# Performance work log

Hardware: AMD Instinct MI355X
Metric: run time of the kernel (lower is better)

## Reference

```python
import jax, jax.numpy as jnp
import numpy as np

B, N = 8192, 64
EPS = 1e-5
KARCHER_STEPS = 1


def _sym_apply(x, fn):
    # f(X) for symmetric X via eigendecomposition: V f(w) V^T
    w, v = jnp.linalg.eigh(x)
    return jnp.einsum('...ij,...j,...kj->...ik', v, fn(w), v)


def _logm(x):
    return _sym_apply(x, jnp.log)


def _expm(x):
    return _sym_apply(x, jnp.exp)


def sym_mat_pow(x, p):
    # X^p for SPD X, scalar (possibly traced) exponent p
    w, v = jnp.linalg.eigh(x)
    return jnp.einsum('...ij,...j,...kj->...ik', v, w ** p, v)


def _sqrt_and_invsqrt(m):
    # single eigh shared between m^{1/2} and m^{-1/2}
    w, v = jnp.linalg.eigh(m)
    sw = jnp.sqrt(w)
    s = jnp.einsum('...ij,...j,...kj->...ik', v, sw, v)
    si = jnp.einsum('...ij,...j,...kj->...ik', v, 1.0 / sw, v)
    return s, si


def karcher_flow(x, steps):
    # Frechet mean under AIRM via Karcher flow, init at arithmetic mean
    mean = x.mean(0)
    for _ in range(steps):
        s, si = _sqrt_and_invsqrt(mean)
        t = _logm(si @ x @ si).mean(0)  # mean tangent at current estimate
        mean = s @ _expm(t) @ s
    return mean


def batch_stats(x):
    mean = karcher_flow(x, KARCHER_STEPS)
    _, si = _sqrt_and_invsqrt(mean)
    logs = _logm(si @ x @ si)  # [B, n, n] tangent vectors at identity
    var = jnp.mean(jnp.sum(logs * logs, axis=(-2, -1)))  # mean squared AIRM distance
    return mean, jnp.sqrt(var)


def setup_inputs() -> dict:
    key = jax.random.key(0)
    k1, k2 = jax.random.split(key, 2)
    g = jax.random.normal(k1, (B, N, N), dtype=jnp.float32)
    x = g @ jnp.swapaxes(g, -1, -2) / N + 1e-3 * jnp.eye(N, dtype=jnp.float32)  # SPD batch
    h = jax.random.normal(k2, (N, N), dtype=jnp.float32)
    shift = h @ h.T / N + 0.1 * jnp.eye(N, dtype=jnp.float32)  # SPD shift parameter
    scale = jnp.ones((1,), dtype=jnp.float32)
    return {"x": x, "shift": shift, "scale": scale}


def reference(x, shift, scale):
    # batch stats are computed under no_grad in torch -> stop_gradient here
    mean, std = batch_stats(x)
    mean = jax.lax.stop_gradient(mean)
    std = jax.lax.stop_gradient(std)

    # parallel transport mean -> identity (whiten): mean^{-1/2} X mean^{-1/2}
    _, mi = _sqrt_and_invsqrt(mean)
    xw = mi @ x @ mi

    # scale by learnable scalar / batch std via matrix power
    p = (scale / (std + EPS))[0]
    y = sym_mat_pow(xw, p)

    # parallel transport identity -> shift: shift^{1/2} Y shift^{1/2}
    ss, _ = _sqrt_and_invsqrt(shift)
    return ss @ y @ ss
```

## Files before the change

### kernel.cpp

```cpp
#include <hip/hip_runtime.h>
#include <math.h>

#define ND 64
#define PAD 65
#define NN 4096
#define NB 8192

#define OFF_MEANPART ((size_t)0)
#define OFF_MEANA    ((size_t)131072)
#define OFF_S        ((size_t)135168)
#define OFF_SI       ((size_t)139264)
#define OFF_SS       ((size_t)143360)
#define OFF_TBAR     ((size_t)147456)
#define OFF_MI       ((size_t)151552)
#define OFF_P        ((size_t)155648)
#define OFF_VARPART  ((size_t)155712)
#define OFF_LAM      ((size_t)156736)
#define OFF_TPART    ((size_t)681024)

__device__ void jacobi2s(float (&A)[ND][PAD], float (&V)[ND][PAD], int tid) {
  __shared__ float cs_[32], sn_[32];
  __shared__ int   pp_[32], qq_[32];
  __shared__ int   rotcnt_;
  __shared__ float fro2_;
  __shared__ float red_[4];

  __syncthreads();
  float loc = 0.f;
  for (int e = tid; e < NN; e += 256) { float a = A[e >> 6][e & 63]; loc += a * a; }
  for (int o = 32; o; o >>= 1) loc += __shfl_down(loc, o);
  if ((tid & 63) == 0) red_[tid >> 6] = loc;
  __syncthreads();
  if (tid == 0) fro2_ = red_[0] + red_[1] + red_[2] + red_[3];
  __syncthreads();
  float fro2 = fro2_;

  for (int sweep = 0; sweep < 20; ++sweep) {
    if (tid == 0) rotcnt_ = 0;
    __syncthreads();
    for (int r = 0; r < 63; ++r) {
      if (tid < 32) {
        int p, q;
        if (tid == 0) { p = 63; q = r; }
        else { p = (r + tid) % 63; q = (r + 63 - tid) % 63; }
        if (p > q) { int t0 = p; p = q; q = t0; }
        pp_[tid] = p; qq_[tid] = q;
        float app = A[p][p], aqq = A[q][q], apq = A[p][q];
        float thr = fmaxf(1e-12f * fabsf(app * aqq), 1e-14f * fro2);
        float c = 1.f, s = 0.f;
        if (apq * apq > thr) {
          float tau = (aqq - app) / (2.f * apq);
          float t = 1.f / (fabsf(tau) + sqrtf(1.f + tau * tau));
          t = (tau < 0.f) ? -t : t;
          c = 1.f / sqrtf(1.f + t * t);
          s = t * c;
          atomicAdd(&rotcnt_, 1);
        }
        cs_[tid] = c; sn_[tid] = s;
      }
      __syncthreads();
      for (int t = tid; t < 2048; t += 256) {
        int k = t >> 6, j = t & 63;
        int p = pp_[k], q = qq_[k]; float c = cs_[k], s = sn_[k];
        float ap = A[p][j], aq = A[q][j];
        A[p][j] = c * ap - s * aq;
        A[q][j] = s * ap + c * aq;
      }
      __syncthreads();
      for (int t = tid; t < 4096; t += 256) {
        int k = (t >> 6) & 31, j = t & 63;
        int p = pp_[k], q = qq_[k]; float c = cs_[k], s = sn_[k];
        if (t < 2048) {
          float ap = A[j][p], aq = A[j][q];
          A[j][p] = c * ap - s * aq;
          A[j][q] = s * ap + c * aq;
        } else {
          float vp = V[j][p], vq = V[j][q];
          V[j][p] = c * vp - s * vq;
          V[j][q] = s * vp + c * vq;
        }
      }
      __syncthreads();
    }
    int rc = rotcnt_;
    __syncthreads();
    if (rc == 0) break;
  }
}

__device__ void recon_write(const float (&V)[ND][PAD], const float* f, float* g,
                            int c, int wq) {
  float acc[16];
#pragma unroll
  for (int k = 0; k < 16; ++k) acc[k] = 0.f;
  for (int j = 0; j < ND; ++j) {
    float m = f[j] * V[c][j];
#pragma unroll
    for (int k = 0; k < 16; ++k) acc[k] = fmaf(V[wq + 4 * k][j], m, acc[k]);
  }
#pragma unroll
  for (int k = 0; k < 16; ++k) g[(wq + 4 * k) * ND + c] = acc[k];
}

__device__ inline void jacobi1s(float (&w)[ND], int lane) {
  float g = 0.f;
#pragma unroll
  for (int i = 0; i < ND; ++i) g = fmaf(w[i], w[i], g);
  for (int sweep = 0; sweep < 18; ++sweep) {
    bool any = false;
    for (int r = 1; r < ND; ++r) {
      int partner = lane ^ r;
      float gv = __shfl(g, partner);
      float v[ND];
#pragma unroll
      for (int i = 0; i < ND; ++i) v[i] = __shfl(w[i], partner);
      float apq = 0.f;
#pragma unroll
      for (int i = 0; i < ND; ++i) apq = fmaf(w[i], v[i], apq);
      if (apq * apq > 4e-10f * g * gv) {
        bool amP = lane < partner;
        float app = amP ? g : gv;
        float aqq = amP ? gv : g;
        float tau = (aqq - app) / (2.f * apq);
        float t = 1.f / (fabsf(tau) + sqrtf(1.f + tau * tau));
        t = (tau < 0.f) ? -t : t;
        float c = 1.f / sqrtf(1.f + t * t);
        float s = t * c;
        float s2 = amP ? -s : s;
#pragma unroll
        for (int i = 0; i < ND; ++i) w[i] = fmaf(s2, v[i], c * w[i]);
        float d = t * apq;
        g = amP ? (g - d) : (g + d);
        any = true;
      }
    }
    if (!__any(any)) break;
  }
}


__global__ __launch_bounds__(256) void k_mean_part(const float* __restrict__ x,
                                                   float* __restrict__ part) {
  int e = blockIdx.x * 256 + threadIdx.x;
  int chunk = blockIdx.y;
  const float* px = x + (size_t)chunk * 256 * NN + e;
  float s = 0.f;
  for (int i = 0; i < 256; ++i) s += px[(size_t)i * NN];
  part[(size_t)chunk * NN + e] = s;
}

__global__ __launch_bounds__(256) void k_mean_final(const float* __restrict__ part,
                                                    float* __restrict__ meanA) {
  int e = blockIdx.x * 256 + threadIdx.x;
  float s = 0.f;
  for (int c = 0; c < 32; ++c) s += part[(size_t)c * NN + e];
  meanA[e] = s * (1.f / (float)NB);
}

__global__ __launch_bounds__(256) void k_prep1(const float* __restrict__ meanA,
                                               const float* __restrict__ shift,
                                               float* __restrict__ s_out,
                                               float* __restrict__ si_out,
                                               float* __restrict__ ss_out) {
  __shared__ float A[ND][PAD], V[ND][PAD];
  __shared__ float f1[ND], f2[ND];
  int tid = threadIdx.x;
  const float* src = (blockIdx.x == 0) ? meanA : shift;
  for (int e = tid; e < NN; e += 256) A[e >> 6][e & 63] = src[e];
  for (int e = tid; e < NN; e += 256) V[e >> 6][e & 63] = ((e >> 6) == (e & 63)) ? 1.f : 0.f;
  jacobi2s(A, V, tid);
  if (tid < ND) {
    float wv = fmaxf(A[tid][tid], 1e-30f);
    f1[tid] = sqrtf(wv);
    f2[tid] = 1.f / sqrtf(wv);
  }
  __syncthreads();
  int c = tid & 63, wq = tid >> 6;
  if (blockIdx.x == 0) {
    recon_write(V, f1, s_out, c, wq);
    recon_write(V, f2, si_out, c, wq);
  } else {
    recon_write(V, f1, ss_out, c, wq);
  }
}

__global__ __launch_bounds__(128, 2) void k_stage2(const float* __restrict__ x,
                                                   const float* __restrict__ si,
                                                   float* __restrict__ tPart,
                                                   int G2) {
  __shared__ float Xs[2][ND][PAD];
  __shared__ float lw_s[2][ND];
  int tid = threadIdx.x;
  int lane = tid & 63;
  int wv = tid >> 6;
  float (&X)[ND][PAD] = Xs[wv];
  int wid = blockIdx.x * 2 + wv;
  int nw = G2 * 2;

  float tacc[ND];
#pragma unroll
  for (int i2 = 0; i2 < ND; ++i2) tacc[i2] = 0.f;

  for (int i = wid; i < NB; i += nw) {
    for (int r2 = 0; r2 < ND; ++r2) X[r2][lane] = x[(size_t)i * NN + r2 * ND + lane];
    float w_[ND];
#pragma unroll
    for (int r2 = 0; r2 < ND; ++r2) w_[r2] = 0.f;
    for (int a = 0; a < ND; ++a) {
      float xa = X[a][lane];
#pragma unroll
      for (int r2 = 0; r2 < ND; ++r2) w_[r2] = fmaf(si[a * ND + r2], xa, w_[r2]);
    }
#pragma unroll
    for (int r2 = 0; r2 < ND; ++r2) X[r2][lane] = w_[r2];
#pragma unroll
    for (int r2 = 0; r2 < ND; ++r2) w_[r2] = 0.f;
    for (int a = 0; a < ND; ++a) {
      float sa = si[a * ND + lane];
#pragma unroll
      for (int r2 = 0; r2 < ND; ++r2) w_[r2] = fmaf(X[r2][a], sa, w_[r2]);
    }
    jacobi1s(w_, lane);
    float s2 = 0.f;
#pragma unroll
    for (int r2 = 0; r2 < ND; ++r2) s2 = fmaf(w_[r2], w_[r2], s2);
    float sig = sqrtf(fmaxf(s2, 1e-38f));
    float inv = 1.f / sig;
    lw_s[wv][lane] = logf(sig);
#pragma unroll
    for (int r2 = 0; r2 < ND; ++r2) X[r2][lane] = w_[r2] * inv;
    for (int j = 0; j < ND; ++j) {
      float m = lw_s[wv][j] * X[lane][j];
#pragma unroll
      for (int r2 = 0; r2 < ND; ++r2) tacc[r2] = fmaf(X[r2][j], m, tacc[r2]);
    }
  }
  if (wv == 1) {
#pragma unroll
    for (int r2 = 0; r2 < ND; ++r2) Xs[1][r2][lane] = tacc[r2];
  }
  __syncthreads();
  if (wv == 0) {
#pragma unroll
    for (int r2 = 0; r2 < ND; ++r2) tacc[r2] += Xs[1][r2][lane];
#pragma unroll
    for (int r2 = 0; r2 < ND; ++r2)
      tPart[(size_t)blockIdx.x * NN + r2 * ND + lane] = tacc[r2];
  }
}

__global__ __launch_bounds__(256) void k_reduce_t(const float* __restrict__ tPart,
                                                  float* __restrict__ tbar, int G2) {
  int e = blockIdx.x * 256 + threadIdx.x;
  float s = 0.f;
  for (int b = 0; b < G2; ++b) s += tPart[(size_t)b * NN + e];
  tbar[e] = s * (1.f / (float)NB);
}

__global__ __launch_bounds__(256) void k_prep2(const float* __restrict__ tbar,
                                               const float* __restrict__ s_g,
                                               float* __restrict__ mi_out) {
  __shared__ float A[ND][PAD], V[ND][PAD];
  __shared__ float f1[ND];
  int tid = threadIdx.x;
  int c = tid & 63, wq = tid >> 6;
  for (int e = tid; e < NN; e += 256) A[e >> 6][e & 63] = tbar[e];
  for (int e = tid; e < NN; e += 256) V[e >> 6][e & 63] = ((e >> 6) == (e & 63)) ? 1.f : 0.f;
  jacobi2s(A, V, tid);
  if (tid < ND) f1[tid] = expf(A[tid][tid]);
  __syncthreads();
  {
    float acc[16];
#pragma unroll
    for (int k = 0; k < 16; ++k) acc[k] = 0.f;
    for (int j = 0; j < ND; ++j) {
      float m = f1[j] * V[c][j];
#pragma unroll
      for (int k = 0; k < 16; ++k) acc[k] = fmaf(V[wq + 4 * k][j], m, acc[k]);
    }
    __syncthreads();
#pragma unroll
    for (int k = 0; k < 16; ++k) A[wq + 4 * k][c] = acc[k];
  }
  __syncthreads();
  {
    float acc[16];
#pragma unroll
    for (int k = 0; k < 16; ++k) acc[k] = 0.f;
    for (int a = 0; a < ND; ++a) {
      float ea = A[a][c];
#pragma unroll
      for (int k = 0; k < 16; ++k) acc[k] = fmaf(s_g[(wq + 4 * k) * ND + a], ea, acc[k]);
    }
    __syncthreads();
#pragma unroll
    for (int k = 0; k < 16; ++k) V[wq + 4 * k][c] = acc[k];
  }
  __syncthreads();
  {
    float acc[16];
#pragma unroll
    for (int k = 0; k < 16; ++k) acc[k] = 0.f;
    for (int a = 0; a < ND; ++a) {
      float sa = s_g[a * ND + c];
#pragma unroll
      for (int k = 0; k < 16; ++k) acc[k] = fmaf(V[wq + 4 * k][a], sa, acc[k]);
    }
    __syncthreads();
#pragma unroll
    for (int k = 0; k < 16; ++k) A[wq + 4 * k][c] = acc[k];
  }
  __syncthreads();
  for (int e = tid; e < NN; e += 256) V[e >> 6][e & 63] = ((e >> 6) == (e & 63)) ? 1.f : 0.f;
  jacobi2s(A, V, tid);
  if (tid < ND) f1[tid] = 1.f / sqrtf(fmaxf(A[tid][tid], 1e-30f));
  __syncthreads();
  recon_write(V, f1, mi_out, c, wq);
}

__global__ __launch_bounds__(128, 2) void k_stage3(const float* __restrict__ x,
                                                   const float* __restrict__ mi,
                                                   const float* __restrict__ ss,
                                                   float* __restrict__ aout,
                                                   float* __restrict__ lam,
                                                   float* __restrict__ varPart) {
  __shared__ float Xs[2][ND][PAD];
  __shared__ float vred[2];
  int tid = threadIdx.x;
  int lane = tid & 63;
  int wv = tid >> 6;
  float (&X)[ND][PAD] = Xs[wv];
  int wid = blockIdx.x * 2 + wv;
  int nw = gridDim.x * 2;
  float varacc = 0.f;

  for (int i = wid; i < NB; i += nw) {
    for (int r2 = 0; r2 < ND; ++r2) X[r2][lane] = x[(size_t)i * NN + r2 * ND + lane];
    float w_[ND];
#pragma unroll
    for (int r2 = 0; r2 < ND; ++r2) w_[r2] = 0.f;
    for (int a = 0; a < ND; ++a) {
      float xa = X[a][lane];
#pragma unroll
      for (int r2 = 0; r2 < ND; ++r2) w_[r2] = fmaf(mi[a * ND + r2], xa, w_[r2]);
    }
#pragma unroll
    for (int r2 = 0; r2 < ND; ++r2) X[r2][lane] = w_[r2];
#pragma unroll
    for (int r2 = 0; r2 < ND; ++r2) w_[r2] = 0.f;
    for (int a = 0; a < ND; ++a) {
      float sa = mi[a * ND + lane];
#pragma unroll
      for (int r2 = 0; r2 < ND; ++r2) w_[r2] = fmaf(X[r2][a], sa, w_[r2]);
    }
    jacobi1s(w_, lane);
    float s2 = 0.f;
#pragma unroll
    for (int r2 = 0; r2 < ND; ++r2) s2 = fmaf(w_[r2], w_[r2], s2);
    float sig = sqrtf(fmaxf(s2, 1e-38f));
    float inv = 1.f / sig;
    lam[(size_t)i * ND + lane] = sig;
    float lg = logf(sig);
    varacc = fmaf(lg, lg, varacc);
#pragma unroll
    for (int r2 = 0; r2 < ND; ++r2) X[r2][lane] = w_[r2] * inv;
    float acc[ND];
#pragma unroll
    for (int r2 = 0; r2 < ND; ++r2) acc[r2] = 0.f;
    for (int a = 0; a < ND; ++a) {
      float ua = X[a][lane];
#pragma unroll
      for (int r2 = 0; r2 < ND; ++r2) acc[r2] = fmaf(ss[a * ND + r2], ua, acc[r2]);
    }
#pragma unroll
    for (int r2 = 0; r2 < ND; ++r2)
      aout[(size_t)i * NN + r2 * ND + lane] = acc[r2];
  }
  for (int o = 32; o; o >>= 1) varacc += __shfl_down(varacc, o);
  if (lane == 0) vred[wv] = varacc;
  __syncthreads();
  if (tid == 0) varPart[blockIdx.x] = vred[0] + vred[1];
}

__global__ __launch_bounds__(64) void k_pfinal(const float* __restrict__ varPart,
                                               const float* __restrict__ scale,
                                               float* __restrict__ pout) {
  int tid = threadIdx.x;
  float s = 0.f;
  for (int i = tid; i < 1024; i += 64) s += varPart[i];
  for (int o = 32; o; o >>= 1) s += __shfl_down(s, o);
  if (tid == 0) {
    float var = s * (1.f / (float)NB);
    float sd = sqrtf(var);
    pout[0] = scale[0] / (sd + 1e-5f);
  }
}

__global__ __launch_bounds__(256) void k_stage5(const float* __restrict__ ain,
                                                const float* __restrict__ lam,
                                                const float* __restrict__ pws,
                                                float* __restrict__ out) {
  __shared__ float Ab[ND][PAD];
  __shared__ float lp[ND];
  int tid = threadIdx.x;
  int i = blockIdx.x;
  for (int e = tid; e < NN; e += 256) Ab[e >> 6][e & 63] = ain[(size_t)i * NN + e];
  if (tid < ND) {
    float p = pws[0];
    lp[tid] = powf(lam[(size_t)i * ND + tid], p);
  }
  __syncthreads();
  int c = tid & 63, wq = tid >> 6;
  float acc[16];
#pragma unroll
  for (int k = 0; k < 16; ++k) acc[k] = 0.f;
  for (int j = 0; j < ND; ++j) {
    float m = lp[j] * Ab[c][j];
#pragma unroll
    for (int k = 0; k < 16; ++k) acc[k] = fmaf(Ab[wq + 4 * k][j], m, acc[k]);
  }
#pragma unroll
  for (int k = 0; k < 16; ++k)
    out[(size_t)i * NN + (wq + 4 * k) * ND + c] = acc[k];
}

extern "C" void kernel_launch(void* const* d_in, const int* in_sizes, int n_in,
                              void* d_out, int out_size, void* d_ws, size_t ws_size,
                              hipStream_t stream) {
  const float* x     = (const float*)d_in[0];
  const float* shift = (const float*)d_in[1];
  const float* scale = (const float*)d_in[2];
  float* out = (float*)d_out;
  float* ws  = (float*)d_ws;
  (void)in_sizes; (void)n_in; (void)out_size;

  size_t wsf = ws_size / 4;
  int G2 = 1024;
  if (OFF_TPART + (size_t)G2 * NN > wsf) {
    size_t avail = (wsf > OFF_TPART) ? (wsf - OFF_TPART) / NN : 1;
    if (avail < 1) avail = 1;
    if (avail < (size_t)G2) G2 = (int)avail;
  }

  k_mean_part<<<dim3(16, 32), 256, 0, stream>>>(x, ws + OFF_MEANPART);
  k_mean_final<<<16, 256, 0, stream>>>(ws + OFF_MEANPART, ws + OFF_MEANA);
  k_prep1<<<2, 256, 0, stream>>>(ws + OFF_MEANA, shift, ws + OFF_S, ws + OFF_SI,
                                 ws + OFF_SS);
  k_stage2<<<G2, 128, 0, stream>>>(x, ws + OFF_SI, ws + OFF_TPART, G2);
  k_reduce_t<<<16, 256, 0, stream>>>(ws + OFF_TPART, ws + OFF_TBAR, G2);
  k_prep2<<<1, 256, 0, stream>>>(ws + OFF_TBAR, ws + OFF_S, ws + OFF_MI);
  k_stage3<<<1024, 128, 0, stream>>>(x, ws + OFF_MI, ws + OFF_SS, out,
                                     ws + OFF_LAM, ws + OFF_VARPART);
  k_pfinal<<<1, 64, 0, stream>>>(ws + OFF_VARPART, scale, ws + OFF_P);
  k_stage5<<<8192, 256, 0, stream>>>(out, ws + OFF_LAM, ws + OFF_P, out);
}
```

Before: 14.77 ms.

## Use DPP lane swaps in one-sided Jacobi and swizzled float4 shared-memory tiles

In the per-matrix one-sided Jacobi, each column-pair exchange now uses DPP row moves, permlane16 swaps and ds_bpermute in place of generic shuffles, and the dot product is split over four accumulators. The congruence transform and the log-reconstruction in stages 2 and 3 now load rows of x with float4 into an XOR-swizzled unpadded shared tile and read it back as float4. The goal is to cut shuffle latency in the hot Jacobi sweeps and reduce LDS bank conflicts and instruction count in the matrix products. In exchange the code is more complex, and it depends on a builtin that may be missing, in which case it falls back to bpermute.

Result: slower. 22.81 ms (+54.4%).

```diff
diff --git a/kernel.cpp b/kernel.cpp
--- a/kernel.cpp
+++ b/kernel.cpp
@@ -17,6 +17,27 @@
 #define OFF_VARPART  ((size_t)155712)
 #define OFF_LAM      ((size_t)156736)
 #define OFF_TPART    ((size_t)681024)
+
+typedef int v2i __attribute__((ext_vector_type(2)));
+
+template<int CTRL>
+__device__ __forceinline__ float dppf(float x) {
+  return __builtin_bit_cast(float,
+      __builtin_amdgcn_mov_dpp(__builtin_bit_cast(int, x), CTRL, 0xF, 0xF, true));
+}
+__device__ __forceinline__ float bperm_f(int pa, float x) {
+  return __builtin_bit_cast(float,
+      __builtin_amdgcn_ds_bpermute(pa, __builtin_bit_cast(int, x)));
+}
+#if __has_builtin(__builtin_amdgcn_permlane16_swap)
+#define HAVE_PL16 1
+__device__ __forceinline__ float pl16x(float x) {
+  int xi = __builtin_bit_cast(int, x);
+  v2i pr = __builtin_amdgcn_permlane16_swap(xi, xi, false, false);
+  unsigned r = (unsigned)pr.x + (unsigned)pr.y - (unsigned)xi;
+  return __builtin_bit_cast(float, (int)r);
+}
+#endif
 
 __device__ void jacobi2s(float (&A)[ND][PAD], float (&V)[ND][PAD], int tid) {
   __shared__ float cs_[32], sn_[32];
@@ -106,18 +127,70 @@
   float g = 0.f;
 #pragma unroll
   for (int i = 0; i < ND; ++i) g = fmaf(w[i], w[i], g);
+
   for (int sweep = 0; sweep < 18; ++sweep) {
     bool any = false;
     for (int r = 1; r < ND; ++r) {
-      int partner = lane ^ r;
-      float gv = __shfl(g, partner);
-      float v[ND];
-#pragma unroll
-      for (int i = 0; i < ND; ++i) v[i] = __shfl(w[i], partner);
-      float apq = 0.f;
-#pragma unroll
-      for (int i = 0; i < ND; ++i) apq = fmaf(w[i], v[i], apq);
+      float v[ND + 1];
+      if (r >= 32) {
+        int pa = ((lane ^ r) << 2);
+#pragma unroll
+        for (int i = 0; i < ND; ++i) v[i] = bperm_f(pa, w[i]);
+        v[ND] = bperm_f(pa, g);
+      } else {
+        switch (r & 3) {
+          case 0:
+#pragma unroll
+            for (int i = 0; i < ND; ++i) v[i] = w[i];
+            v[ND] = g;
+            break;
+          case 1:
+#pragma unroll
+            for (int i = 0; i < ND; ++i) v[i] = dppf<0xB1>(w[i]);
+            v[ND] = dppf<0xB1>(g);
+            break;
+          case 2:
+#pragma unroll
+            for (int i = 0; i < ND; ++i) v[i] = dppf<0x4E>(w[i]);
+            v[ND] = dppf<0x4E>(g);
+            break;
+          default:
+#pragma unroll
+            for (int i = 0; i < ND; ++i) v[i] = dppf<0x1B>(w[i]);
+            v[ND] = dppf<0x1B>(g);
+            break;
+        }
+        if (r & 4) {
+#pragma unroll
+          for (int i = 0; i <= ND; ++i) v[i] = dppf<0x1B>(dppf<0x141>(v[i]));
+        }
+        if (r & 8) {
+#pragma unroll
+          for (int i = 0; i <= ND; ++i) v[i] = dppf<0x141>(dppf<0x140>(v[i]));
+        }
+        if (r & 16) {
+#ifdef HAVE_PL16
+#pragma unroll
+          for (int i = 0; i <= ND; ++i) v[i] = pl16x(v[i]);
+#else
+          int pa16 = ((lane ^ 16) << 2);
+#pragma unroll
+          for (int i = 0; i <= ND; ++i) v[i] = bperm_f(pa16, v[i]);
+#endif
+        }
+      }
+      float gv = v[ND];
+      float a0 = 0.f, a1 = 0.f, a2 = 0.f, a3 = 0.f;
+#pragma unroll
+      for (int i = 0; i < ND; i += 4) {
+        a0 = fmaf(w[i + 0], v[i + 0], a0);
+        a1 = fmaf(w[i + 1], v[i + 1], a1);
+        a2 = fmaf(w[i + 2], v[i + 2], a2);
+        a3 = fmaf(w[i + 3], v[i + 3], a3);
+      }
+      float apq = (a0 + a1) + (a2 + a3);
       if (apq * apq > 4e-10f * g * gv) {
+        int partner = lane ^ r;
         bool amP = lane < partner;
         float app = amP ? g : gv;
         float aqq = amP ? gv : g;
@@ -138,6 +211,40 @@
   }
 }
 
+__device__ inline void congruence(const float* __restrict__ x_i,
+                                  const float* __restrict__ si,
+                                  float* __restrict__ XL, int lane,
+                                  float (&w_)[ND]) {
+#pragma unroll
+  for (int k = 0; k < 16; ++k) {
+    float4 rv = ((const float4*)(x_i + lane * ND))[k];
+    ((float4*)(XL + lane * ND))[k ^ (lane & 7)] = rv;
+  }
+  float B[ND];
+#pragma unroll
+  for (int i = 0; i < ND; ++i) B[i] = 0.f;
+  for (int a = 0; a < ND; ++a) {
+    float sa = si[a * ND + lane];
+    int ro = a * ND, sw = a & 7;
+#pragma unroll
+    for (int k = 0; k < 16; ++k) {
+      const float4 c4 = *((const float4*)(XL + ro + ((k ^ sw) << 2)));
+      B[4 * k + 0] = fmaf(c4.x, sa, B[4 * k + 0]);
+      B[4 * k + 1] = fmaf(c4.y, sa, B[4 * k + 1]);
+      B[4 * k + 2] = fmaf(c4.z, sa, B[4 * k + 2]);
+      B[4 * k + 3] = fmaf(c4.w, sa, B[4 * k + 3]);
+    }
+  }
+#pragma unroll
+  for (int a = 0; a < ND; ++a) XL[a * ND + lane] = B[a];
+#pragma unroll
+  for (int i = 0; i < ND; ++i) w_[i] = 0.f;
+  for (int a = 0; a < ND; ++a) {
+    float ba = XL[a * ND + lane];
+#pragma unroll
+    for (int r2 = 0; r2 < ND; ++r2) w_[r2] = fmaf(si[a * ND + r2], ba, w_[r2]);
+  }
+}
 
 __global__ __launch_bounds__(256) void k_mean_part(const float* __restrict__ x,
                                                    float* __restrict__ part) {
@@ -188,61 +295,58 @@
                                                    const float* __restrict__ si,
                                                    float* __restrict__ tPart,
                                                    int G2) {
-  __shared__ float Xs[2][ND][PAD];
-  __shared__ float lw_s[2][ND];
-  int tid = threadIdx.x;
-  int lane = tid & 63;
-  int wv = tid >> 6;
-  float (&X)[ND][PAD] = Xs[wv];
+  __shared__ float XLs[2][NN];
+  __shared__ float lws[2][ND];
+  int tid = threadIdx.x, lane = tid & 63, wv = tid >> 6;
+  float* XL = XLs[wv];
   int wid = blockIdx.x * 2 + wv;
   int nw = G2 * 2;
 
   float tacc[ND];
 #pragma unroll
-  for (int i2 = 0; i2 < ND; ++i2) tacc[i2] = 0.f;
+  for (int i = 0; i < ND; ++i) tacc[i] = 0.f;
 
   for (int i = wid; i < NB; i += nw) {
-    for (int r2 = 0; r2 < ND; ++r2) X[r2][lane] = x[(size_t)i * NN + r2 * ND + lane];
     float w_[ND];
-#pragma unroll
-    for (int r2 = 0; r2 < ND; ++r2) w_[r2] = 0.f;
-    for (int a = 0; a < ND; ++a) {
-      float xa = X[a][lane];
-#pragma unroll
-      for (int r2 = 0; r2 < ND; ++r2) w_[r2] = fmaf(si[a * ND + r2], xa, w_[r2]);
-    }
-#pragma unroll
-    for (int r2 = 0; r2 < ND; ++r2) X[r2][lane] = w_[r2];
-#pragma unroll
-    for (int r2 = 0; r2 < ND; ++r2) w_[r2] = 0.f;
-    for (int a = 0; a < ND; ++a) {
-      float sa = si[a * ND + lane];
-#pragma unroll
-      for (int r2 = 0; r2 < ND; ++r2) w_[r2] = fmaf(X[r2][a], sa, w_[r2]);
-    }
+    congruence(x + (size_t)i * NN, si, XL, lane, w_);
     jacobi1s(w_, lane);
     float s2 = 0.f;
 #pragma unroll
     for (int r2 = 0; r2 < ND; ++r2) s2 = fmaf(w_[r2], w_[r2], s2);
     float sig = sqrtf(fmaxf(s2, 1e-38f));
     float inv = 1.f / sig;
-    lw_s[wv][lane] = logf(sig);
-#pragma unroll
-    for (int r2 = 0; r2 < ND; ++r2) X[r2][lane] = w_[r2] * inv;
+    lws[wv][lane] = logf(sig);
+#pragma unroll
+    for (int k = 0; k < 16; ++k) {
+      float4 uv;
+      uv.x = w_[4 * k + 0] * inv;
+      uv.y = w_[4 * k + 1] * inv;
+      uv.z = w_[4 * k + 2] * inv;
+      uv.w = w_[4 * k + 3] * inv;
+      ((float4*)(XL + lane * ND))[k ^ (lane & 7)] = uv;
+    }
     for (int j = 0; j < ND; ++j) {
-      float m = lw_s[wv][j] * X[lane][j];
-#pragma unroll
-      for (int r2 = 0; r2 < ND; ++r2) tacc[r2] = fmaf(X[r2][j], m, tacc[r2]);
+      int ro = j * ND, sw = j & 7;
+      float uj = XL[ro + (((lane >> 2) ^ sw) << 2) + (lane & 3)];
+      float m = lws[wv][j] * uj;
+#pragma unroll
+      for (int k = 0; k < 16; ++k) {
+        const float4 c4 = *((const float4*)(XL + ro + ((k ^ sw) << 2)));
+        tacc[4 * k + 0] = fmaf(c4.x, m, tacc[4 * k + 0]);
+        tacc[4 * k + 1] = fmaf(c4.y, m, tacc[4 * k + 1]);
+        tacc[4 * k + 2] = fmaf(c4.z, m, tacc[4 * k + 2]);
+        tacc[4 * k + 3] = fmaf(c4.w, m, tacc[4 * k + 3]);
+      }
     }
   }
   if (wv == 1) {
 #pragma unroll
-    for (int r2 = 0; r2 < ND; ++r2) Xs[1][r2][lane] = tacc[r2];
+    for (int r2 = 0; r2 < ND; ++r2) XLs[1][r2 * ND + lane] = tacc[r2];
   }
   __syncthreads();
   if (wv == 0) {
 #pragma unroll
-    for (int r2 = 0; r2 < ND; ++r2) tacc[r2] += Xs[1][r2][lane];
+    for (int r2 = 0; r2 < ND; ++r2) tacc[r2] += XLs[1][r2 * ND + lane];
 #pragma unroll
     for (int r2 = 0; r2 < ND; ++r2)
       tPart[(size_t)blockIdx.x * NN + r2 * ND + lane] = tacc[r2];
@@ -324,35 +428,17 @@
                                                    float* __restrict__ aout,
                                                    float* __restrict__ lam,
                                                    float* __restrict__ varPart) {
-  __shared__ float Xs[2][ND][PAD];
+  __shared__ float XLs[2][NN];
   __shared__ float vred[2];
-  int tid = threadIdx.x;
-  int lane = tid & 63;
-  int wv = tid >> 6;
-  float (&X)[ND][PAD] = Xs[wv];
+  int tid = threadIdx.x, lane = tid & 63, wv = tid >> 6;
+  float* XL = XLs[wv];
   int wid = blockIdx.x * 2 + wv;
   int nw = gridDim.x * 2;
   float varacc = 0.f;
 
   for (int i = wid; i < NB; i += nw) {
-    for (int r2 = 0; r2 < ND; ++r2) X[r2][lane] = x[(size_t)i * NN + r2 * ND + lane];
     float w_[ND];
-#pragma unroll
-    for (int r2 = 0; r2 < ND; ++r2) w_[r2] = 0.f;
-    for (int a = 0; a < ND; ++a) {
-      float xa = X[a][lane];
-#pragma unroll
-      for (int r2 = 0; r2 < ND; ++r2) w_[r2] = fmaf(mi[a * ND + r2], xa, w_[r2]);
-    }
-#pragma unroll
-    for (int r2 = 0; r2 < ND; ++r2) X[r2][lane] = w_[r2];
-#pragma unroll
-    for (int r2 = 0; r2 < ND; ++r2) w_[r2] = 0.f;
-    for (int a = 0; a < ND; ++a) {
-      float sa = mi[a * ND + lane];
-#pragma unroll
-      for (int r2 = 0; r2 < ND; ++r2) w_[r2] = fmaf(X[r2][a], sa, w_[r2]);
-    }
+    congruence(x + (size_t)i * NN, mi, XL, lane, w_);
     jacobi1s(w_, lane);
     float s2 = 0.f;
 #pragma unroll
@@ -363,12 +449,12 @@
     float lg = logf(sig);
     varacc = fmaf(lg, lg, varacc);
 #pragma unroll
-    for (int r2 = 0; r2 < ND; ++r2) X[r2][lane] = w_[r2] * inv;
+    for (int a = 0; a < ND; ++a) XL[a * ND + lane] = w_[a] * inv;
     float acc[ND];
 #pragma unroll
     for (int r2 = 0; r2 < ND; ++r2) acc[r2] = 0.f;
     for (int a = 0; a < ND; ++a) {
-      float ua = X[a][lane];
+      float ua = XL[a * ND + lane];
 #pragma unroll
       for (int r2 = 0; r2 < ND; ++r2) acc[r2] = fmaf(ss[a * ND + r2], ua, acc[r2]);
     }
```

## Restructure per-matrix stages to one wave per block with swizzled LDS and bpermute Jacobi

Applied to the files above, without the earlier changes.

Stage 2 and stage 3 now run one 64-lane wave per block with twice as many blocks, each using a 16 KB unpadded LDS tile with an XOR swizzle so rows can be read and written as float4 without bank conflicts. The congruence products read the matrix in vectorized form and split accumulations across four FMA chains. The one-sided Jacobi sweep exchanges partner columns through ds_bpermute, with the norm folded into the same exchange, and returns the final column norm directly. Workspace offsets and the partial-reduction counts are adjusted for the larger grid. This adds more partial tiles to reduce and more LDS per block.

After: 16.29 ms. 10.3% more time.

```diff
diff --git a/kernel.cpp b/kernel.cpp
--- a/kernel.cpp
+++ b/kernel.cpp
@@ -15,8 +15,128 @@
 #define OFF_MI       ((size_t)151552)
 #define OFF_P        ((size_t)155648)
 #define OFF_VARPART  ((size_t)155712)
-#define OFF_LAM      ((size_t)156736)
-#define OFF_TPART    ((size_t)681024)
+#define OFF_LAM      ((size_t)157760)
+#define OFF_TPART    ((size_t)682048)
+
+#define G2_BLOCKS 2048
+#define G3_BLOCKS 2048
+
+__device__ __forceinline__ float bperm_f(int pa, float x) {
+  return __builtin_bit_cast(float,
+      __builtin_amdgcn_ds_bpermute(pa, __builtin_bit_cast(int, x)));
+}
+
+__device__ __forceinline__ constexpr int skey(int row) { return (row + (row >> 4)) & 15; }
+__device__ __forceinline__ int swz4(int row, int g) { return row * 64 + ((g ^ skey(row)) << 2); }
+__device__ __forceinline__ int swzE(int row, int e) {
+  return row * 64 + (((e >> 2) ^ skey(row)) << 2) + (e & 3);
+}
+
+__device__ float jacobi1s64(float (&w)[ND], int lane) {
+  float a0 = 0.f, a1 = 0.f, a2 = 0.f, a3 = 0.f;
+#pragma unroll
+  for (int i = 0; i < ND; i += 4) {
+    a0 = fmaf(w[i + 0], w[i + 0], a0);
+    a1 = fmaf(w[i + 1], w[i + 1], a1);
+    a2 = fmaf(w[i + 2], w[i + 2], a2);
+    a3 = fmaf(w[i + 3], w[i + 3], a3);
+  }
+  float g = (a0 + a1) + (a2 + a3);
+
+  for (int sweep = 0; sweep < 18; ++sweep) {
+    bool any = false;
+    for (int r = 1; r < ND; ++r) {
+      int pa = (lane ^ r) << 2;
+      float v[ND + 1];
+#pragma unroll
+      for (int i = 0; i <= ND; ++i) {
+        float t = bperm_f(pa, (i < ND) ? w[i] : g);
+        asm volatile("" : "+v"(t));
+        v[i] = t;
+      }
+      float gv = v[ND];
+      float b0 = 0.f, b1 = 0.f, b2 = 0.f, b3 = 0.f;
+#pragma unroll
+      for (int i = 0; i < ND; i += 4) {
+        b0 = fmaf(w[i + 0], v[i + 0], b0);
+        b1 = fmaf(w[i + 1], v[i + 1], b1);
+        b2 = fmaf(w[i + 2], v[i + 2], b2);
+        b3 = fmaf(w[i + 3], v[i + 3], b3);
+      }
+      float apq = (b0 + b1) + (b2 + b3);
+      if (apq * apq > 4e-10f * g * gv) {
+        int partner = lane ^ r;
+        bool amP = lane < partner;
+        float app = amP ? g : gv;
+        float aqq = amP ? gv : g;
+        float tau = (aqq - app) / (2.f * apq);
+        float t = 1.f / (fabsf(tau) + sqrtf(1.f + tau * tau));
+        t = (tau < 0.f) ? -t : t;
+        float c = 1.f / sqrtf(1.f + t * t);
+        float s = t * c;
+        float s2v = amP ? -s : s;
+#pragma unroll
+        for (int i = 0; i < ND; ++i) w[i] = fmaf(s2v, v[i], c * w[i]);
+        float d = t * apq;
+        g = amP ? (g - d) : (g + d);
+        any = true;
+      }
+    }
+    if (!__any(any)) break;
+  }
+  a0 = a1 = a2 = a3 = 0.f;
+#pragma unroll
+  for (int i = 0; i < ND; i += 4) {
+    a0 = fmaf(w[i + 0], w[i + 0], a0);
+    a1 = fmaf(w[i + 1], w[i + 1], a1);
+    a2 = fmaf(w[i + 2], w[i + 2], a2);
+    a3 = fmaf(w[i + 3], w[i + 3], a3);
+  }
+  return (a0 + a1) + (a2 + a3);
+}
+
+__device__ __forceinline__ void congruence1(const float* __restrict__ xi,
+                                            const float* __restrict__ q,
+                                            float* __restrict__ Xb, int lane,
+                                            float (&w)[ND]) {
+#pragma unroll
+  for (int k = 0; k < 16; ++k) {
+    int flat = k * 256 + lane * 4;
+    float4 rv = *(const float4*)(xi + flat);
+    int a = flat >> 6;
+    *(float4*)(Xb + swz4(a, lane & 15)) = rv;
+  }
+  __syncthreads();
+  float B[ND];
+#pragma unroll
+  for (int r = 0; r < ND; ++r) B[r] = 0.f;
+  const float* qc = q + lane * ND;
+  for (int a = 0; a < ND; ++a) {
+    float sa = qc[a];
+#pragma unroll
+    for (int g2 = 0; g2 < 16; ++g2) {
+      float4 xa = *(const float4*)(Xb + swz4(a, g2));
+      B[4 * g2 + 0] = fmaf(xa.x, sa, B[4 * g2 + 0]);
+      B[4 * g2 + 1] = fmaf(xa.y, sa, B[4 * g2 + 1]);
+      B[4 * g2 + 2] = fmaf(xa.z, sa, B[4 * g2 + 2]);
+      B[4 * g2 + 3] = fmaf(xa.w, sa, B[4 * g2 + 3]);
+    }
+  }
+  __syncthreads();
+#pragma unroll
+  for (int g2 = 0; g2 < 16; ++g2) {
+    float4 b4 = make_float4(B[4 * g2 + 0], B[4 * g2 + 1], B[4 * g2 + 2], B[4 * g2 + 3]);
+    *(float4*)(Xb + swz4(lane, g2)) = b4;
+  }
+#pragma unroll
+  for (int r = 0; r < ND; ++r) w[r] = 0.f;
+  for (int a = 0; a < ND; ++a) {
+    float ba = Xb[swzE(lane, a)];
+    const float* qr = q + a * ND;
+#pragma unroll
+    for (int r = 0; r < ND; ++r) w[r] = fmaf(qr[r], ba, w[r]);
+  }
+}
 
 __device__ void jacobi2s(float (&A)[ND][PAD], float (&V)[ND][PAD], int tid) {
   __shared__ float cs_[32], sn_[32];
@@ -102,43 +222,6 @@
   for (int k = 0; k < 16; ++k) g[(wq + 4 * k) * ND + c] = acc[k];
 }
 
-__device__ inline void jacobi1s(float (&w)[ND], int lane) {
-  float g = 0.f;
-#pragma unroll
-  for (int i = 0; i < ND; ++i) g = fmaf(w[i], w[i], g);
-  for (int sweep = 0; sweep < 18; ++sweep) {
-    bool any = false;
-    for (int r = 1; r < ND; ++r) {
-      int partner = lane ^ r;
-      float gv = __shfl(g, partner);
-      float v[ND];
-#pragma unroll
-      for (int i = 0; i < ND; ++i) v[i] = __shfl(w[i], partner);
-      float apq = 0.f;
-#pragma unroll
-      for (int i = 0; i < ND; ++i) apq = fmaf(w[i], v[i], apq);
-      if (apq * apq > 4e-10f * g * gv) {
-        bool amP = lane < partner;
-        float app = amP ? g : gv;
-        float aqq = amP ? gv : g;
-        float tau = (aqq - app) / (2.f * apq);
-        float t = 1.f / (fabsf(tau) + sqrtf(1.f + tau * tau));
-        t = (tau < 0.f) ? -t : t;
-        float c = 1.f / sqrtf(1.f + t * t);
-        float s = t * c;
-        float s2 = amP ? -s : s;
-#pragma unroll
-        for (int i = 0; i < ND; ++i) w[i] = fmaf(s2, v[i], c * w[i]);
-        float d = t * apq;
-        g = amP ? (g - d) : (g + d);
-        any = true;
-      }
-    }
-    if (!__any(any)) break;
-  }
-}
-
-
 __global__ __launch_bounds__(256) void k_mean_part(const float* __restrict__ x,
                                                    float* __restrict__ part) {
   int e = blockIdx.x * 256 + threadIdx.x;
@@ -184,76 +267,56 @@
   }
 }
 
-__global__ __launch_bounds__(128, 2) void k_stage2(const float* __restrict__ x,
-                                                   const float* __restrict__ si,
-                                                   float* __restrict__ tPart,
-                                                   int G2) {
-  __shared__ float Xs[2][ND][PAD];
-  __shared__ float lw_s[2][ND];
-  int tid = threadIdx.x;
-  int lane = tid & 63;
-  int wv = tid >> 6;
-  float (&X)[ND][PAD] = Xs[wv];
-  int wid = blockIdx.x * 2 + wv;
-  int nw = G2 * 2;
+__global__ __launch_bounds__(64, 1) void k_stage2(const float* __restrict__ x,
+                                                  const float* __restrict__ si,
+                                                  float* __restrict__ tPart,
+                                                  int G2) {
+  __shared__ float Xb[4096];
+  int lane = threadIdx.x;
 
   float tacc[ND];
 #pragma unroll
-  for (int i2 = 0; i2 < ND; ++i2) tacc[i2] = 0.f;
-
-  for (int i = wid; i < NB; i += nw) {
-    for (int r2 = 0; r2 < ND; ++r2) X[r2][lane] = x[(size_t)i * NN + r2 * ND + lane];
-    float w_[ND];
-#pragma unroll
-    for (int r2 = 0; r2 < ND; ++r2) w_[r2] = 0.f;
-    for (int a = 0; a < ND; ++a) {
-      float xa = X[a][lane];
-#pragma unroll
-      for (int r2 = 0; r2 < ND; ++r2) w_[r2] = fmaf(si[a * ND + r2], xa, w_[r2]);
-    }
-#pragma unroll
-    for (int r2 = 0; r2 < ND; ++r2) X[r2][lane] = w_[r2];
-#pragma unroll
-    for (int r2 = 0; r2 < ND; ++r2) w_[r2] = 0.f;
-    for (int a = 0; a < ND; ++a) {
-      float sa = si[a * ND + lane];
-#pragma unroll
-      for (int r2 = 0; r2 < ND; ++r2) w_[r2] = fmaf(X[r2][a], sa, w_[r2]);
-    }
-    jacobi1s(w_, lane);
-    float s2 = 0.f;
-#pragma unroll
-    for (int r2 = 0; r2 < ND; ++r2) s2 = fmaf(w_[r2], w_[r2], s2);
+  for (int i = 0; i < ND; ++i) tacc[i] = 0.f;
+
+  for (int i = blockIdx.x; i < NB; i += G2) {
+    __syncthreads();
+    float w[ND];
+    congruence1(x + (size_t)i * NN, si, Xb, lane, w);
+    float s2 = jacobi1s64(w, lane);
     float sig = sqrtf(fmaxf(s2, 1e-38f));
     float inv = 1.f / sig;
-    lw_s[wv][lane] = logf(sig);
-#pragma unroll
-    for (int r2 = 0; r2 < ND; ++r2) X[r2][lane] = w_[r2] * inv;
+    float lg = logf(sig);
+#pragma unroll
+    for (int g2 = 0; g2 < 16; ++g2) {
+      float4 u4 = make_float4(w[4 * g2 + 0] * inv, w[4 * g2 + 1] * inv,
+                              w[4 * g2 + 2] * inv, w[4 * g2 + 3] * inv);
+      *(float4*)(Xb + swz4(lane, g2)) = u4;
+    }
+    __syncthreads();
     for (int j = 0; j < ND; ++j) {
-      float m = lw_s[wv][j] * X[lane][j];
-#pragma unroll
-      for (int r2 = 0; r2 < ND; ++r2) tacc[r2] = fmaf(X[r2][j], m, tacc[r2]);
-    }
-  }
-  if (wv == 1) {
-#pragma unroll
-    for (int r2 = 0; r2 < ND; ++r2) Xs[1][r2][lane] = tacc[r2];
-  }
-  __syncthreads();
-  if (wv == 0) {
-#pragma unroll
-    for (int r2 = 0; r2 < ND; ++r2) tacc[r2] += Xs[1][r2][lane];
-#pragma unroll
-    for (int r2 = 0; r2 < ND; ++r2)
-      tPart[(size_t)blockIdx.x * NN + r2 * ND + lane] = tacc[r2];
-  }
+      float lwj = __shfl(lg, j);
+      float uj = Xb[swzE(j, lane)];
+      float m = lwj * uj;
+#pragma unroll
+      for (int g2 = 0; g2 < 16; ++g2) {
+        float4 u4 = *(const float4*)(Xb + swz4(j, g2));
+        tacc[4 * g2 + 0] = fmaf(u4.x, m, tacc[4 * g2 + 0]);
+        tacc[4 * g2 + 1] = fmaf(u4.y, m, tacc[4 * g2 + 1]);
+        tacc[4 * g2 + 2] = fmaf(u4.z, m, tacc[4 * g2 + 2]);
+        tacc[4 * g2 + 3] = fmaf(u4.w, m, tacc[4 * g2 + 3]);
+      }
+    }
+  }
+#pragma unroll
+  for (int r = 0; r < ND; ++r)
+    tPart[(size_t)blockIdx.x * NN + r * ND + lane] = tacc[r];
 }
 
 __global__ __launch_bounds__(256) void k_reduce_t(const float* __restrict__ tPart,
-                                                  float* __restrict__ tbar, int G2) {
+                                                  float* __restrict__ tbar, int nw) {
   int e = blockIdx.x * 256 + threadIdx.x;
   float s = 0.f;
-  for (int b = 0; b < G2; ++b) s += tPart[(size_t)b * NN + e];
+  for (int b = 0; b < nw; ++b) s += tPart[(size_t)b * NN + e];
   tbar[e] = s * (1.f / (float)NB);
 }
 
@@ -318,76 +381,56 @@
   recon_write(V, f1, mi_out, c, wq);
 }
 
-__global__ __launch_bounds__(128, 2) void k_stage3(const float* __restrict__ x,
-                                                   const float* __restrict__ mi,
-                                                   const float* __restrict__ ss,
-                                                   float* __restrict__ aout,
-                                                   float* __restrict__ lam,
-                                                   float* __restrict__ varPart) {
-  __shared__ float Xs[2][ND][PAD];
-  __shared__ float vred[2];
-  int tid = threadIdx.x;
-  int lane = tid & 63;
-  int wv = tid >> 6;
-  float (&X)[ND][PAD] = Xs[wv];
-  int wid = blockIdx.x * 2 + wv;
-  int nw = gridDim.x * 2;
+__global__ __launch_bounds__(64, 1) void k_stage3(const float* __restrict__ x,
+                                                  const float* __restrict__ mi,
+                                                  const float* __restrict__ ss,
+                                                  float* __restrict__ aout,
+                                                  float* __restrict__ lam,
+                                                  float* __restrict__ varPart,
+                                                  int G3) {
+  __shared__ float Xb[4096];
+  int lane = threadIdx.x;
   float varacc = 0.f;
 
-  for (int i = wid; i < NB; i += nw) {
-    for (int r2 = 0; r2 < ND; ++r2) X[r2][lane] = x[(size_t)i * NN + r2 * ND + lane];
-    float w_[ND];
-#pragma unroll
-    for (int r2 = 0; r2 < ND; ++r2) w_[r2] = 0.f;
-    for (int a = 0; a < ND; ++a) {
-      float xa = X[a][lane];
-#pragma unroll
-      for (int r2 = 0; r2 < ND; ++r2) w_[r2] = fmaf(mi[a * ND + r2], xa, w_[r2]);
-    }
-#pragma unroll
-    for (int r2 = 0; r2 < ND; ++r2) X[r2][lane] = w_[r2];
-#pragma unroll
-    for (int r2 = 0; r2 < ND; ++r2) w_[r2] = 0.f;
-    for (int a = 0; a < ND; ++a) {
-      float sa = mi[a * ND + lane];
-#pragma unroll
-      for (int r2 = 0; r2 < ND; ++r2) w_[r2] = fmaf(X[r2][a], sa, w_[r2]);
-    }
-    jacobi1s(w_, lane);
-    float s2 = 0.f;
-#pragma unroll
-    for (int r2 = 0; r2 < ND; ++r2) s2 = fmaf(w_[r2], w_[r2], s2);
+  for (int i = blockIdx.x; i < NB; i += G3) {
+    __syncthreads();
+    float w[ND];
+    congruence1(x + (size_t)i * NN, mi, Xb, lane, w);
+    float s2 = jacobi1s64(w, lane);
     float sig = sqrtf(fmaxf(s2, 1e-38f));
     float inv = 1.f / sig;
     lam[(size_t)i * ND + lane] = sig;
     float lg = logf(sig);
     varacc = fmaf(lg, lg, varacc);
 #pragma unroll
-    for (int r2 = 0; r2 < ND; ++r2) X[r2][lane] = w_[r2] * inv;
+    for (int g2 = 0; g2 < 16; ++g2) {
+      float4 u4 = make_float4(w[4 * g2 + 0] * inv, w[4 * g2 + 1] * inv,
+                              w[4 * g2 + 2] * inv, w[4 * g2 + 3] * inv);
+      *(float4*)(Xb + swz4(lane, g2)) = u4;
+    }
     float acc[ND];
 #pragma unroll
-    for (int r2 = 0; r2 < ND; ++r2) acc[r2] = 0.f;
+    for (int r = 0; r < ND; ++r) acc[r] = 0.f;
     for (int a = 0; a < ND; ++a) {
-      float ua = X[a][lane];
-#pragma unroll
-      for (int r2 = 0; r2 < ND; ++r2) acc[r2] = fmaf(ss[a * ND + r2], ua, acc[r2]);
-    }
-#pragma unroll
-    for (int r2 = 0; r2 < ND; ++r2)
-      aout[(size_t)i * NN + r2 * ND + lane] = acc[r2];
+      float ua = Xb[swzE(lane, a)];
+      const float* ssr = ss + a * ND;
+#pragma unroll
+      for (int r = 0; r < ND; ++r) acc[r] = fmaf(ssr[r], ua, acc[r]);
+    }
+#pragma unroll
+    for (int r = 0; r < ND; ++r)
+      aout[(size_t)i * NN + r * ND + lane] = acc[r];
   }
   for (int o = 32; o; o >>= 1) varacc += __shfl_down(varacc, o);
-  if (lane == 0) vred[wv] = varacc;
-  __syncthreads();
-  if (tid == 0) varPart[blockIdx.x] = vred[0] + vred[1];
+  if (lane == 0) varPart[blockIdx.x] = varacc;
 }
 
 __global__ __launch_bounds__(64) void k_pfinal(const float* __restrict__ varPart,
                                                const float* __restrict__ scale,
-                                               float* __restrict__ pout) {
+                                               float* __restrict__ pout, int n) {
   int tid = threadIdx.x;
   float s = 0.f;
-  for (int i = tid; i < 1024; i += 64) s += varPart[i];
+  for (int i = tid; i < n; i += 64) s += varPart[i];
   for (int o = 32; o; o >>= 1) s += __shfl_down(s, o);
   if (tid == 0) {
     float var = s * (1.f / (float)NB);
@@ -435,7 +478,7 @@
   (void)in_sizes; (void)n_in; (void)out_size;
 
   size_t wsf = ws_size / 4;
-  int G2 = 1024;
+  int G2 = G2_BLOCKS;
   if (OFF_TPART + (size_t)G2 * NN > wsf) {
     size_t avail = (wsf > OFF_TPART) ? (wsf - OFF_TPART) / NN : 1;
     if (avail < 1) avail = 1;
@@ -446,11 +489,11 @@
   k_mean_final<<<16, 256, 0, stream>>>(ws + OFF_MEANPART, ws + OFF_MEANA);
   k_prep1<<<2, 256, 0, stream>>>(ws + OFF_MEANA, shift, ws + OFF_S, ws + OFF_SI,
                                  ws + OFF_SS);
-  k_stage2<<<G2, 128, 0, stream>>>(x, ws + OFF_SI, ws + OFF_TPART, G2);
+  k_stage2<<<G2, 64, 0, stream>>>(x, ws + OFF_SI, ws + OFF_TPART, G2);
   k_reduce_t<<<16, 256, 0, stream>>>(ws + OFF_TPART, ws + OFF_TBAR, G2);
   k_prep2<<<1, 256, 0, stream>>>(ws + OFF_TBAR, ws + OFF_S, ws + OFF_MI);
-  k_stage3<<<1024, 128, 0, stream>>>(x, ws + OFF_MI, ws + OFF_SS, out,
-                                     ws + OFF_LAM, ws + OFF_VARPART);
-  k_pfinal<<<1, 64, 0, stream>>>(ws + OFF_VARPART, scale, ws + OFF_P);
+  k_stage3<<<G3_BLOCKS, 64, 0, stream>>>(x, ws + OFF_MI, ws + OFF_SS, out,
+                                         ws + OFF_LAM, ws + OFF_VARPART, G3_BLOCKS);
+  k_pfinal<<<1, 64, 0, stream>>>(ws + OFF_VARPART, scale, ws + OFF_P, G3_BLOCKS);
   k_stage5<<<8192, 256, 0, stream>>>(out, ws + OFF_LAM, ws + OFF_P, out);
 }
```
